# Performance work log

Measured on AMD Instinct MI355X. Metric: run time of the kernel, lower is better.

Reference implementation:

```python
import jax, jax.numpy as jnp
import numpy as np

N_NODES = 50000
D = 512
N_EDGES = 1600000

def setup_inputs() -> dict:
    key = jax.random.key(0)
    ks = jax.random.split(key, 5)
    x = jax.random.normal(ks[0], (N_NODES, D), dtype=jnp.float32)
    W = jax.random.normal(ks[1], (D, D), dtype=jnp.float32) * (1.0 / np.sqrt(D))
    b = jnp.zeros((D,), dtype=jnp.float32)
    edge_weight = jax.random.uniform(ks[2], (N_EDGES,), dtype=jnp.float32)
    edge_src = jax.random.randint(ks[3], (N_EDGES,), 0, N_NODES, dtype=jnp.int32)
    edge_dst = jax.random.randint(ks[4], (N_EDGES,), 0, N_NODES, dtype=jnp.int32)
    return {"x": x, "W": W, "b": b, "edge_weight": edge_weight,
            "edge_src": edge_src, "edge_dst": edge_dst}

def reference(x, W, b, edge_weight, edge_src, edge_dst):
    # GraphConvolution: support = x @ W; out = spmm(adj, support) + b
    support = x @ W                                  # [N, D] dense GEMM
    msgs = support[edge_src] * edge_weight[:, None]  # gather + scale [E, D]
    agg = jax.ops.segment_sum(msgs, edge_dst, num_segments=x.shape[0])  # [N, D]
    gc_out = agg + b
    # GCN2: relu then residual
    return jax.nn.relu(gc_out) + x
```

## Files before the change

### kernel.cpp

```cpp
#include <hip/hip_runtime.h>

#define N_NODES 50000
#define DIM 512
#define N_EDGES 1600000
#define CHSHIFT 12
#define NCHUNK 13
#define CAPC 20
#define DPW 12
#define NWAVE 4167

typedef __attribute__((ext_vector_type(8))) short short8;
typedef __attribute__((ext_vector_type(8))) unsigned short ushort8;
typedef __attribute__((ext_vector_type(4))) float floatx4;
typedef __attribute__((ext_vector_type(8))) _Float16 half8;

__device__ __forceinline__ unsigned short f2bf(float v) {
    unsigned u = __float_as_uint(v);
    unsigned r = u + 0x7FFF + ((u >> 16) & 1);
    return (unsigned short)(r >> 16);
}
__device__ __forceinline__ float bf2f(unsigned short h) {
    return __uint_as_float((unsigned)h << 16);
}
__device__ __forceinline__ void stage16(const char* g, char* l) {
    __builtin_amdgcn_global_load_lds((const __attribute__((address_space(1))) void*)g,
                                     (__attribute__((address_space(3))) void*)l, 16, 0, 0);
}

__global__ __launch_bounds__(256) void convert_x(const float* __restrict__ x,
                                                 _Float16* __restrict__ xh) {
    const int t = blockIdx.x * 256 + threadIdx.x;
    if (t >= N_NODES * 64) return;
    const int row = t >> 6;
    const int kc = t & 63;
    const int blk = kc >> 3;
    const int c = kc & 7;
    const int cSw = c ^ (row & 7);

    const floatx4 v0 = __builtin_nontemporal_load((const floatx4*)&x[row * DIM + kc * 8]);
    const floatx4 v1 = __builtin_nontemporal_load((const floatx4*)&x[row * DIM + kc * 8 + 4]);
    const float v[8] = {v0.x, v0.y, v0.z, v0.w, v1.x, v1.y, v1.z, v1.w};
    half8 h;
#pragma unroll
    for (int j = 0; j < 8; j++) h[j] = (_Float16)v[j];
    *(half8*)&xh[row * DIM + blk * 64 + cSw * 8] = h;
}

__global__ __launch_bounds__(256) void convert_w(const float* __restrict__ W,
                                                 _Float16* __restrict__ wh) {
    const int t = blockIdx.x * 256 + threadIdx.x;
    if (t >= DIM * 64) return;
    const int n = t >> 6;
    const int kc = t & 63;
    const int blk = kc >> 3;
    const int c = kc & 7;
    const int cSw = c ^ (n & 7);

    half8 h;
#pragma unroll
    for (int j = 0; j < 8; j++) h[j] = (_Float16)W[(kc * 8 + j) * DIM + n];
    *(half8*)&wh[n * DIM + blk * 64 + cSw * 8] = h;
}

__global__ __launch_bounds__(256, 3) void gemm_f16(const _Float16* __restrict__ A,
                                                   const _Float16* __restrict__ B,
                                                   _Float16* __restrict__ Cb, int M) {
    __shared__ __align__(128) char smem[32768];

    const int tid = threadIdx.x;
    const int row0 = blockIdx.y * 128;
    const int col0 = blockIdx.x * 128;

    int srow[4], schk[4];
#pragma unroll
    for (int i = 0; i < 4; i++) {
        const int q = i * 256 + tid;
        srow[i] = q >> 3;
        schk[i] = q & 7;
    }

    const int l = tid & 63;
    const int w = tid >> 6;
    const int wm = w & 1, wn = w >> 1;
    const int lrow = l & 15;
    const int kg = l >> 4;
    const int s = l & 7;

    int offA[4][2], offB[4][2];
#pragma unroll
    for (int mt = 0; mt < 4; mt++)
#pragma unroll
        for (int h = 0; h < 2; h++) {
            const int chunk = (kg + 4 * h) ^ s;
            offA[mt][h] = (wm * 64 + mt * 16 + lrow) * 128 + chunk * 16;
            offB[mt][h] = 16384 + (wn * 64 + mt * 16 + lrow) * 128 + chunk * 16;
        }

    floatx4 acc[4][4];
#pragma unroll
    for (int i = 0; i < 4; i++)
#pragma unroll
        for (int j = 0; j < 4; j++) acc[i][j] = (floatx4)(0.f);

    const char* A8 = (const char*)A;
    const char* B8 = (const char*)B;

    for (int kblk = 0; kblk < 8; kblk++) {
        __syncthreads();
#pragma unroll
        for (int i = 0; i < 4; i++) {
            const int q16 = (i * 256 + tid) * 16;
            const size_t ga = (size_t)min(row0 + srow[i], M - 1) * (DIM * 2)
                              + kblk * 128 + schk[i] * 16;
            const size_t gb = (size_t)(col0 + srow[i]) * (DIM * 2)
                              + kblk * 128 + schk[i] * 16;
            stage16(A8 + ga, smem + q16);
            stage16(B8 + gb, smem + 16384 + q16);
        }
        __syncthreads();

#pragma unroll
        for (int h = 0; h < 2; h++) {
            half8 bf[4];
#pragma unroll
            for (int nt = 0; nt < 4; nt++) bf[nt] = *(const half8*)(smem + offB[nt][h]);
#pragma unroll
            for (int mt = 0; mt < 4; mt++) {
                const half8 af = *(const half8*)(smem + offA[mt][h]);
#pragma unroll
                for (int nt = 0; nt < 4; nt++)
                    acc[mt][nt] = __builtin_amdgcn_mfma_f32_16x16x32_f16(
                        af, bf[nt], acc[mt][nt], 0, 0, 0);
            }
        }
    }

    const int crow0 = row0 + wm * 64;
    const int ccol0 = col0 + wn * 64;
#pragma unroll
    for (int mt = 0; mt < 4; mt++) {
        const int rbase = crow0 + mt * 16 + kg * 4;
#pragma unroll
        for (int nt = 0; nt < 4; nt++) {
            const int cc = ccol0 + nt * 16 + lrow;
#pragma unroll
            for (int r = 0; r < 4; r++) {
                const int gr = rbase + r;
                if (gr < M) Cb[(size_t)gr * DIM + cc] = (_Float16)acc[mt][nt][r];
            }
        }
    }
}

__global__ __launch_bounds__(256) void gcn_build_edges(const int* __restrict__ esrc,
                                                       const int* __restrict__ edst,
                                                       const float* __restrict__ ew,
                                                       int* __restrict__ cursor,
                                                       unsigned int* __restrict__ table) {
    const int e = blockIdx.x * 256 + threadIdx.x;
    if (e >= N_EDGES) return;
    const int d = __builtin_nontemporal_load(&edst[e]);
    const int s = __builtin_nontemporal_load(&esrc[e]);
    const float w = __builtin_nontemporal_load(&ew[e]);
    const int ch = s >> CHSHIFT;
    const int pos = atomicAdd(&cursor[ch * N_NODES + d], 1);
    if (pos < CAPC) {
        const unsigned rec = (unsigned)s | ((unsigned)f2bf(w) << 16);
        __builtin_nontemporal_store(
            rec, &table[((size_t)ch * N_NODES + d) * CAPC + pos]);
    }
}

__global__ __launch_bounds__(256) void gcn_pack_counts(const int* __restrict__ cursor,
                                                       unsigned char* __restrict__ pcntT) {
    const int c = blockIdx.y;
    const int w = blockIdx.x * 256 + threadIdx.x;
    if (w >= NWAVE) return;
    unsigned wd[4] = {0, 0, 0, 0};
#pragma unroll
    for (int k = 0; k < DPW; k++) {
        const int dst = w * DPW + k;
        const unsigned cnt = (dst < N_NODES)
            ? (unsigned)min(cursor[c * N_NODES + dst], CAPC) : 0u;
        wd[k >> 2] |= cnt << ((k & 3) * 8);
    }
    uint4 o; o.x = wd[0]; o.y = wd[1]; o.z = wd[2]; o.w = wd[3];
    *(uint4*)(pcntT + ((size_t)c * NWAVE + w) * 16) = o;
}

__global__ __launch_bounds__(64, 4) void gcn_aggregate_pers(
        const _Float16* __restrict__ sup,
        const unsigned char* __restrict__ pcntT,
        const unsigned int* __restrict__ table,
        const _Float16* __restrict__ xh,
        const float* __restrict__ b,
        float* __restrict__ out) {
    const int blk = blockIdx.x;
    const int tid = threadIdx.x;
    const int c8 = tid * 8;

    float acc[DPW][8];
#pragma unroll
    for (int k = 0; k < DPW; k++)
#pragma unroll
        for (int j = 0; j < 8; j++) acc[k][j] = 0.f;

    const _Float16* supc = sup + c8;

    for (int c = 0; c < NCHUNK; c++) {
        const uint4 pcv = *(const uint4*)(pcntT + ((size_t)c * NWAVE + blk) * 16);
        const unsigned pw[4] = {pcv.x, pcv.y, pcv.z, pcv.w};
#pragma unroll
        for (int k = 0; k < DPW; k++) {
            const int dst = blk * DPW + k;
            const int cnt = (int)((pw[k >> 2] >> ((k & 3) * 8)) & 0xFFu);
            const size_t segbase = ((size_t)c * N_NODES + dst) * CAPC;
#pragma unroll 2
            for (int i = 0; i < cnt; i++) {
                const unsigned rec = table[segbase + i];
                const float wt = bf2f((unsigned short)(rec >> 16));
                const half8 v = *(const half8*)(supc + (size_t)(rec & 0xFFFFu) * DIM);
#pragma unroll
                for (int j = 0; j < 8; j++)
                    acc[k][j] = fmaf(wt, (float)v[j], acc[k][j]);
            }
        }
        asm volatile("" ::: "memory");
    }

    const float4 b0 = *(const float4*)&b[c8];
    const float4 b1 = *(const float4*)&b[c8 + 4];
    const float bb[8] = {b0.x, b0.y, b0.z, b0.w, b1.x, b1.y, b1.z, b1.w};
#pragma unroll
    for (int k = 0; k < DPW; k++) {
        const int n = blk * DPW + k;
        if (n >= N_NODES) continue;
        const int xoff = n * DIM + (tid >> 3) * 64 + (((tid & 7) ^ (n & 7)) * 8);
        const half8 xb = *(const half8*)&xh[xoff];
        float o[8];
#pragma unroll
        for (int j = 0; j < 8; j++)
            o[j] = fmaxf(acc[k][j] + bb[j], 0.f) + (float)xb[j];
        floatx4 o0, o1;
        o0.x = o[0]; o0.y = o[1]; o0.z = o[2]; o0.w = o[3];
        o1.x = o[4]; o1.y = o[5]; o1.z = o[6]; o1.w = o[7];
        __builtin_nontemporal_store(o0, (floatx4*)&out[(size_t)n * DIM + c8]);
        __builtin_nontemporal_store(o1, (floatx4*)&out[(size_t)n * DIM + c8 + 4]);
    }
}

extern "C" void kernel_launch(void* const* d_in, const int* in_sizes, int n_in,
                              void* d_out, int out_size, void* d_ws, size_t ws_size,
                              hipStream_t stream) {
    const float* x = (const float*)d_in[0];
    const float* W = (const float*)d_in[1];
    const float* b = (const float*)d_in[2];
    const float* ew = (const float*)d_in[3];
    const int* esrc = (const int*)d_in[4];
    const int* edst = (const int*)d_in[5];
    float* out = (float*)d_out;

    char* ws = (char*)d_ws;
    size_t off = 0;
    _Float16* support = (_Float16*)(ws + off);       off += (size_t)N_NODES * DIM * 2;
    int* cursor = (int*)(ws + off);                  off += (size_t)NCHUNK * N_NODES * 4;
    unsigned int* table = (unsigned int*)(ws + off); off += (size_t)NCHUNK * N_NODES * CAPC * 4;
    unsigned char* pcntT = (unsigned char*)(ws + off); off += (size_t)NCHUNK * NWAVE * 16;
    _Float16* xh = (_Float16*)(ws + off);            off += (size_t)N_NODES * DIM * 2;
    _Float16* wh = (_Float16*)(ws + off);            off += (size_t)DIM * DIM * 2;

    (void)hipMemsetAsync(cursor, 0, (size_t)NCHUNK * N_NODES * sizeof(int), stream);

    convert_w<<<(DIM * 64 + 255) / 256, 256, 0, stream>>>(W, wh);
    convert_x<<<(N_NODES * 64 + 255) / 256, 256, 0, stream>>>(x, xh);

    gcn_build_edges<<<(N_EDGES + 255) / 256, 256, 0, stream>>>(esrc, edst, ew,
                                                               cursor, table);
    dim3 pack_grid((NWAVE + 255) / 256, NCHUNK);
    gcn_pack_counts<<<pack_grid, 256, 0, stream>>>(cursor, pcntT);

    dim3 gemm_grid(DIM / 128, (N_NODES + 127) / 128);
    gemm_f16<<<gemm_grid, 256, 0, stream>>>(xh, wh, support, N_NODES);

    gcn_aggregate_pers<<<NWAVE, 64, 0, stream>>>(support, pcntT, table, xh, b, out);
}
```

Baseline: 675.6 us.

## Coarsen source chunks, stride node assignment, drop count-pack kernel, add tail kernel

Source-node chunking goes from 13 chunks of 4096 to 4 chunks of 16384, with per-segment capacity raised to 40. The aggregation kernel now reads edge counts straight from the cursor array, so the separate count-packing kernel is removed. Each 64-thread block handles nodes strided by 4096 instead of 12 contiguous nodes, and a new tail kernel covers the remaining 848 nodes. The aim is fewer chunk iterations, one fewer launch, and better load balance, at the cost of a larger working set per chunk and more scattered count loads.

```diff
diff --git a/kernel.cpp b/kernel.cpp
--- a/kernel.cpp
+++ b/kernel.cpp
@@ -3,14 +3,14 @@
 #define N_NODES 50000
 #define DIM 512
 #define N_EDGES 1600000
-#define CHSHIFT 12
-#define NCHUNK 13
-#define CAPC 20
+#define CHSHIFT 14
+#define NCHUNK 4
+#define CAPC 40
+#define PBLK 4096
 #define DPW 12
-#define NWAVE 4167
+#define TAIL (N_NODES - PBLK * DPW)
 
 typedef __attribute__((ext_vector_type(8))) short short8;
-typedef __attribute__((ext_vector_type(8))) unsigned short ushort8;
 typedef __attribute__((ext_vector_type(4))) float floatx4;
 typedef __attribute__((ext_vector_type(8))) _Float16 half8;
 
@@ -171,31 +171,31 @@
     }
 }
 
-__global__ __launch_bounds__(256) void gcn_pack_counts(const int* __restrict__ cursor,
-                                                       unsigned char* __restrict__ pcntT) {
-    const int c = blockIdx.y;
-    const int w = blockIdx.x * 256 + threadIdx.x;
-    if (w >= NWAVE) return;
-    unsigned wd[4] = {0, 0, 0, 0};
-#pragma unroll
-    for (int k = 0; k < DPW; k++) {
-        const int dst = w * DPW + k;
-        const unsigned cnt = (dst < N_NODES)
-            ? (unsigned)min(cursor[c * N_NODES + dst], CAPC) : 0u;
-        wd[k >> 2] |= cnt << ((k & 3) * 8);
-    }
-    uint4 o; o.x = wd[0]; o.y = wd[1]; o.z = wd[2]; o.w = wd[3];
-    *(uint4*)(pcntT + ((size_t)c * NWAVE + w) * 16) = o;
+__device__ __forceinline__ void write_node(int n, int tid, const float* acc,
+                                           const float* bb,
+                                           const _Float16* __restrict__ xh,
+                                           float* __restrict__ out) {
+    const int c8 = tid * 8;
+    const int xoff = n * DIM + (tid >> 3) * 64 + (((tid & 7) ^ (n & 7)) * 8);
+    const half8 xb = *(const half8*)&xh[xoff];
+    float o[8];
+#pragma unroll
+    for (int j = 0; j < 8; j++) o[j] = fmaxf(acc[j] + bb[j], 0.f) + (float)xb[j];
+    floatx4 o0, o1;
+    o0.x = o[0]; o0.y = o[1]; o0.z = o[2]; o0.w = o[3];
+    o1.x = o[4]; o1.y = o[5]; o1.z = o[6]; o1.w = o[7];
+    __builtin_nontemporal_store(o0, (floatx4*)&out[(size_t)n * DIM + c8]);
+    __builtin_nontemporal_store(o1, (floatx4*)&out[(size_t)n * DIM + c8 + 4]);
 }
 
 __global__ __launch_bounds__(64, 4) void gcn_aggregate_pers(
         const _Float16* __restrict__ sup,
-        const unsigned char* __restrict__ pcntT,
+        const int* __restrict__ cursor,
         const unsigned int* __restrict__ table,
         const _Float16* __restrict__ xh,
         const float* __restrict__ b,
         float* __restrict__ out) {
-    const int blk = blockIdx.x;
+    const int w = blockIdx.x;
     const int tid = threadIdx.x;
     const int c8 = tid * 8;
 
@@ -208,12 +208,10 @@
     const _Float16* supc = sup + c8;
 
     for (int c = 0; c < NCHUNK; c++) {
-        const uint4 pcv = *(const uint4*)(pcntT + ((size_t)c * NWAVE + blk) * 16);
-        const unsigned pw[4] = {pcv.x, pcv.y, pcv.z, pcv.w};
 #pragma unroll
         for (int k = 0; k < DPW; k++) {
-            const int dst = blk * DPW + k;
-            const int cnt = (int)((pw[k >> 2] >> ((k & 3) * 8)) & 0xFFu);
+            const int dst = w + k * PBLK;
+            const int cnt = min(cursor[c * N_NODES + dst], CAPC);
             const size_t segbase = ((size_t)c * N_NODES + dst) * CAPC;
 #pragma unroll 2
             for (int i = 0; i < cnt; i++) {
@@ -232,21 +230,44 @@
     const float4 b1 = *(const float4*)&b[c8 + 4];
     const float bb[8] = {b0.x, b0.y, b0.z, b0.w, b1.x, b1.y, b1.z, b1.w};
 #pragma unroll
-    for (int k = 0; k < DPW; k++) {
-        const int n = blk * DPW + k;
-        if (n >= N_NODES) continue;
-        const int xoff = n * DIM + (tid >> 3) * 64 + (((tid & 7) ^ (n & 7)) * 8);
-        const half8 xb = *(const half8*)&xh[xoff];
-        float o[8];
-#pragma unroll
-        for (int j = 0; j < 8; j++)
-            o[j] = fmaxf(acc[k][j] + bb[j], 0.f) + (float)xb[j];
-        floatx4 o0, o1;
-        o0.x = o[0]; o0.y = o[1]; o0.z = o[2]; o0.w = o[3];
-        o1.x = o[4]; o1.y = o[5]; o1.z = o[6]; o1.w = o[7];
-        __builtin_nontemporal_store(o0, (floatx4*)&out[(size_t)n * DIM + c8]);
-        __builtin_nontemporal_store(o1, (floatx4*)&out[(size_t)n * DIM + c8 + 4]);
-    }
+    for (int k = 0; k < DPW; k++)
+        write_node(w + k * PBLK, tid, acc[k], bb, xh, out);
+}
+
+__global__ __launch_bounds__(64) void gcn_aggregate_tail(
+        const _Float16* __restrict__ sup,
+        const int* __restrict__ cursor,
+        const unsigned int* __restrict__ table,
+        const _Float16* __restrict__ xh,
+        const float* __restrict__ b,
+        float* __restrict__ out) {
+    const int n = PBLK * DPW + blockIdx.x;
+    const int tid = threadIdx.x;
+    const int c8 = tid * 8;
+
+    float acc[8];
+#pragma unroll
+    for (int j = 0; j < 8; j++) acc[j] = 0.f;
+
+    const _Float16* supc = sup + c8;
+
+    for (int c = 0; c < NCHUNK; c++) {
+        const int cnt = min(cursor[c * N_NODES + n], CAPC);
+        const size_t segbase = ((size_t)c * N_NODES + n) * CAPC;
+#pragma unroll 2
+        for (int i = 0; i < cnt; i++) {
+            const unsigned rec = table[segbase + i];
+            const float wt = bf2f((unsigned short)(rec >> 16));
+            const half8 v = *(const half8*)(supc + (size_t)(rec & 0xFFFFu) * DIM);
+#pragma unroll
+            for (int j = 0; j < 8; j++) acc[j] = fmaf(wt, (float)v[j], acc[j]);
+        }
+    }
+
+    const float4 b0 = *(const float4*)&b[c8];
+    const float4 b1 = *(const float4*)&b[c8 + 4];
+    const float bb[8] = {b0.x, b0.y, b0.z, b0.w, b1.x, b1.y, b1.z, b1.w};
+    write_node(n, tid, acc, bb, xh, out);
 }
 
 extern "C" void kernel_launch(void* const* d_in, const int* in_sizes, int n_in,
@@ -265,7 +286,6 @@
     _Float16* support = (_Float16*)(ws + off);       off += (size_t)N_NODES * DIM * 2;
     int* cursor = (int*)(ws + off);                  off += (size_t)NCHUNK * N_NODES * 4;
     unsigned int* table = (unsigned int*)(ws + off); off += (size_t)NCHUNK * N_NODES * CAPC * 4;
-    unsigned char* pcntT = (unsigned char*)(ws + off); off += (size_t)NCHUNK * NWAVE * 16;
     _Float16* xh = (_Float16*)(ws + off);            off += (size_t)N_NODES * DIM * 2;
     _Float16* wh = (_Float16*)(ws + off);            off += (size_t)DIM * DIM * 2;
 
@@ -276,11 +296,10 @@
 
     gcn_build_edges<<<(N_EDGES + 255) / 256, 256, 0, stream>>>(esrc, edst, ew,
                                                                cursor, table);
-    dim3 pack_grid((NWAVE + 255) / 256, NCHUNK);
-    gcn_pack_counts<<<pack_grid, 256, 0, stream>>>(cursor, pcntT);
 
     dim3 gemm_grid(DIM / 128, (N_NODES + 127) / 128);
     gemm_f16<<<gemm_grid, 256, 0, stream>>>(xh, wh, support, N_NODES);
 
-    gcn_aggregate_pers<<<NWAVE, 64, 0, stream>>>(support, pcntT, table, xh, b, out);
-}
+    gcn_aggregate_pers<<<PBLK, 64, 0, stream>>>(support, cursor, table, xh, b, out);
+    gcn_aggregate_tail<<<TAIL, 64, 0, stream>>>(support, cursor, table, xh, b, out);
+}
```

Measured after the change: 578.1 us. 1.17x faster.
